# Performance work log

Measured on AMD Instinct MI355X. Metric: run time of the kernel, lower is better.

The kernel has to match this reference:

```python
import jax, jax.numpy as jnp
import numpy as np

B, T, D = 1024, 20, 50          # batch sessions, seq len (hardcoded 20), emb dim (hardcoded 50)
S1S2 = 50 * 20                  # sample1 * sample2 friend nodes (GAT src)
DEG = 50                        # avg in-degree per dst node
E = B * DEG
NUM_USERS, NUM_ITEMS = 100000, 50000


def _lstm(x, W_ih, W_hh, b_ih, b_hh):
    """PyTorch-style LSTM (gate order i,f,g,o). x: [N,T,D] -> hs: [T,N,D]."""
    N = x.shape[0]
    h0 = jnp.zeros((N, x.shape[-1]), x.dtype)
    def step(carry, xt):
        h, c = carry
        gates = xt @ W_ih.T + h @ W_hh.T + b_ih + b_hh
        i, f, g, o = jnp.split(gates, 4, axis=-1)
        c = jax.nn.sigmoid(f) * c + jax.nn.sigmoid(i) * jnp.tanh(g)
        h = jax.nn.sigmoid(o) * jnp.tanh(c)
        return (h, c), h
    (_, _), hs = jax.lax.scan(step, (h0, h0), jnp.swapaxes(x, 0, 1))
    return hs


def _gat(feat_src, feat_dst, edge_src, edge_dst, fc_W, fc_b):
    """u_dot_v -> edge_softmax (per dst) -> u_mul_e_sum -> relu(fc)."""
    n_dst = feat_dst.shape[0]
    src_e = feat_src[edge_src]                           # [E, D] gather
    score = jnp.sum(src_e * feat_dst[edge_dst], axis=-1) # [E] u_dot_v
    m = jax.ops.segment_max(score, edge_dst, num_segments=n_dst)
    ex = jnp.exp(score - m[edge_dst])
    den = jax.ops.segment_sum(ex, edge_dst, num_segments=n_dst)
    w = ex / den[edge_dst]                               # edge_softmax
    agg = jax.ops.segment_sum(w[:, None] * src_e, edge_dst, num_segments=n_dst)
    return jax.nn.relu(agg @ fc_W.T + fc_b)


def setup_inputs() -> dict:
    key = jax.random.key(0)
    ks = jax.random.split(key, 16)
    input_session = jax.random.randint(ks[0], (B, T), 0, NUM_ITEMS, dtype=jnp.int32)
    support_nodes_layer1 = jax.random.randint(ks[1], (S1S2,), 0, NUM_USERS, dtype=jnp.int32)
    support_sessions_layer1 = jax.random.randint(ks[2], (S1S2, T), 0, NUM_ITEMS, dtype=jnp.int32)
    edge_src = jax.random.randint(ks[3], (E,), 0, S1S2, dtype=jnp.int32)
    edge_dst = jnp.repeat(jnp.arange(B, dtype=jnp.int32), DEG)  # every dst has DEG edges
    s = 0.05
    user_emb = jax.random.normal(ks[4], (NUM_USERS, D), jnp.float32) * s
    item_emb = (jax.random.normal(ks[5], (NUM_ITEMS, D), jnp.float32) * s).at[0].set(0.0)  # padding_idx=0
    W_ih = jax.random.normal(ks[6], (4 * D, D), jnp.float32) * s
    W_hh = jax.random.normal(ks[7], (4 * D, D), jnp.float32) * s
    b_ih = jax.random.normal(ks[8], (4 * D,), jnp.float32) * s
    b_hh = jax.random.normal(ks[9], (4 * D,), jnp.float32) * s
    W1 = jax.random.normal(ks[10], (D, 2 * D), jnp.float32) * s
    fc_W = jax.random.normal(ks[11], (D, D), jnp.float32) * s
    fc_b = jax.random.normal(ks[12], (D,), jnp.float32) * s
    W2 = jax.random.normal(ks[13], (D, 3 * D), jnp.float32) * s
    return {"input_session": input_session, "support_nodes_layer1": support_nodes_layer1,
            "support_sessions_layer1": support_sessions_layer1, "edge_src": edge_src,
            "edge_dst": edge_dst, "user_emb": user_emb, "item_emb": item_emb,
            "W_ih": W_ih, "W_hh": W_hh, "b_ih": b_ih, "b_hh": b_hh,
            "W1": W1, "fc_W": fc_W, "fc_b": fc_b, "W2": W2}


def reference(input_session, support_nodes_layer1, support_sessions_layer1, edge_src, edge_dst,
              user_emb, item_emb, W_ih, W_hh, b_ih, b_hh, W1, fc_W, fc_b, W2):
    # current-user short-term: LSTM over session item embeddings, take last hidden
    output = _lstm(item_emb[input_session], W_ih, W_hh, b_ih, b_hh)[-1]        # [B, D]
    # friends long-term (user emb) + short-term (LSTM over friend sessions, step 0 as in source)
    long_term1 = user_emb[support_nodes_layer1]                                 # [S1S2, D]
    short_term1 = _lstm(item_emb[support_sessions_layer1], W_ih, W_hh, b_ih, b_hh)[0]  # [S1S2, D]
    ls1 = jax.nn.relu(jnp.concatenate([long_term1, short_term1], axis=-1) @ W1.T)      # [S1S2, D]
    # GAT: gather -> per-dst edge softmax -> scatter weighted sum
    gat_out = _gat(ls1, output, edge_src, edge_dst, fc_W, fc_b)                 # [B, D]
    feat = jnp.concatenate([output, gat_out], axis=-1)                          # [B, 2D]
    sr = jnp.concatenate([output, feat], axis=-1) @ W2.T                        # [B, D]
    logits = sr @ item_emb[1:].T                                                # [B, NUM_ITEMS-1]
    return logits
```

## Files before the change

kernel.cpp:

```cpp
#include <hip/hip_runtime.h>
#include <math.h>

#define D 50
#define T 20
#define BATCH 1024
#define S1S2 1000
#define DEG 50
#define NITEMS 50000
#define NLOGITS 49999
#define KPAD 64
#define SLAB 64
#define CHW 64
#define NCHN 784
#define NIPAD (NCHN * CHW)
#define LROWI 66
#define PREP_BLKS ((NIPAD * (KPAD / 2) + 255) / 256)

using bf16x8 = __attribute__((ext_vector_type(8))) __bf16;
using f32x4  = __attribute__((ext_vector_type(4))) float;

__device__ __forceinline__ float sigf(float x) { return 1.0f / (1.0f + expf(-x)); }

__device__ __forceinline__ unsigned short f2bf(float f) {
    unsigned u = __builtin_bit_cast(unsigned, f);
    u = (u + 0x7FFFu + ((u >> 16) & 1u)) >> 16;
    return (unsigned short)u;
}

__global__ __launch_bounds__(256) void fused_front_kernel(
    const int* __restrict__ sess,
    const int* __restrict__ nodes,
    const int* __restrict__ fsess,
    const float* __restrict__ user_emb,
    const float* __restrict__ item_emb,
    const float* __restrict__ W_ih,
    const float* __restrict__ W_hh,
    const float* __restrict__ b_ih,
    const float* __restrict__ b_hh,
    const float* __restrict__ W1,
    float* __restrict__ out_h,
    float* __restrict__ ls1,
    unsigned* __restrict__ item_u)
{
    const int blk = blockIdx.x;
    const int t = threadIdx.x;

    if (blk < BATCH) {
        const int b = blk;
        __shared__ float x_s[D];
        __shared__ float h_s[D];
        __shared__ float g_s[4 * D];
        __shared__ int idx_s[T];

        if (t < T) idx_s[t] = sess[b * T + t];

        float wih[D], whh[D];
        float bias = 0.f;
        if (t < 4 * D) {
            #pragma unroll
            for (int k = 0; k < D; ++k) {
                wih[k] = W_ih[t * D + k];
                whh[k] = W_hh[t * D + k];
            }
            bias = b_ih[t] + b_hh[t];
        }
        float c = 0.f;
        if (t < D) h_s[t] = 0.f;
        __syncthreads();
        if (t < D) x_s[t] = item_emb[(size_t)idx_s[0] * D + t];
        __syncthreads();

        for (int step = 0; step < T; ++step) {
            float xn = 0.f;
            if (t < D && step + 1 < T)
                xn = item_emb[(size_t)idx_s[step + 1] * D + t];
            if (t < 4 * D) {
                float g = bias;
                #pragma unroll
                for (int k = 0; k < D; ++k)
                    g += wih[k] * x_s[k] + whh[k] * h_s[k];
                g_s[t] = g;
            }
            __syncthreads();
            if (t < D) {
                float ig = sigf(g_s[t]);
                float fg = sigf(g_s[D + t]);
                float gg = tanhf(g_s[2 * D + t]);
                float og = sigf(g_s[3 * D + t]);
                c = fg * c + ig * gg;
                h_s[t] = og * tanhf(c);
                if (step + 1 < T) x_s[t] = xn;
            }
            __syncthreads();
        }
        if (t < D) out_h[b * D + t] = h_s[t];
    } else if (blk < BATCH + S1S2) {
        const int s = blk - BATCH;
        __shared__ float fx_s[D];
        __shared__ float fh_s[D];
        __shared__ float fg_s[4 * D];

        if (t < D) fx_s[t] = item_emb[(size_t)fsess[s * T] * D + t];
        __syncthreads();
        if (t < 4 * D) {
            float g = b_ih[t] + b_hh[t];
            #pragma unroll
            for (int k = 0; k < D; ++k) g += W_ih[t * D + k] * fx_s[k];
            fg_s[t] = g;
        }
        __syncthreads();
        if (t < D) {
            float ig = sigf(fg_s[t]);
            float gg = tanhf(fg_s[2 * D + t]);
            float og = sigf(fg_s[3 * D + t]);
            float c1 = ig * gg;
            fh_s[t] = og * tanhf(c1);
        }
        __syncthreads();
        if (t < D) {
            const int node = nodes[s];
            const float* ue = user_emb + (size_t)node * D;
            const float* w1r = W1 + t * 2 * D;
            float acc = 0.f;
            #pragma unroll
            for (int k = 0; k < D; ++k) acc += ue[k] * w1r[k];
            #pragma unroll
            for (int k = 0; k < D; ++k) acc += fh_s[k] * w1r[D + k];
            ls1[s * D + t] = fmaxf(acc, 0.f);
        }
    } else {
        const int idx = (blk - BATCH - S1S2) * 256 + t;
        if (idx >= NIPAD * (KPAD / 2)) return;
        const int r = idx >> 5, c2 = idx & 31;
        const int c0 = c2 * 2, c1 = c0 + 1;
        float f0 = 0.f, f1 = 0.f;
        if (r < NLOGITS) {
            const float* row = item_emb + (size_t)(1 + r) * D;
            if (c0 < D) f0 = row[c0];
            if (c1 < D) f1 = row[c1];
        }
        item_u[idx] = (unsigned)f2bf(f0) | ((unsigned)f2bf(f1) << 16);
    }
}

__global__ __launch_bounds__(64) void gat_sr_kernel(
    const float* __restrict__ out_h,
    const float* __restrict__ ls1,
    const int* __restrict__ edge_src,
    const float* __restrict__ fc_W,
    const float* __restrict__ fc_b,
    const float* __restrict__ W2,
    unsigned* __restrict__ sr_u)
{
    const int b = blockIdx.x;
    const int l = threadIdx.x;
    __shared__ float q[D];
    __shared__ int srcs[DEG];
    __shared__ float w_s[DEG];
    __shared__ float a_s[D];
    __shared__ float g_s[D];
    __shared__ float srow_s[KPAD];

    srow_s[l] = 0.f;
    if (l < D) q[l] = out_h[b * D + l];
    if (l < DEG) srcs[l] = edge_src[b * DEG + l];
    __syncthreads();

    float sc = -INFINITY;
    if (l < DEG) {
        const float* row = ls1 + (size_t)srcs[l] * D;
        float s = 0.f;
        #pragma unroll
        for (int k = 0; k < D; ++k) s += row[k] * q[k];
        sc = s;
    }
    float m = sc;
    #pragma unroll
    for (int off = 32; off; off >>= 1) m = fmaxf(m, __shfl_xor(m, off));
    float ex = (l < DEG) ? expf(sc - m) : 0.f;
    float den = ex;
    #pragma unroll
    for (int off = 32; off; off >>= 1) den += __shfl_xor(den, off);
    if (l < DEG) w_s[l] = ex / den;
    __syncthreads();

    if (l < D) {
        float a = 0.f;
        #pragma unroll
        for (int j = 0; j < DEG; ++j) a += w_s[j] * ls1[(size_t)srcs[j] * D + l];
        a_s[l] = a;
    }
    __syncthreads();
    if (l < D) {
        float g = fc_b[l];
        #pragma unroll
        for (int k = 0; k < D; ++k) g += a_s[k] * fc_W[l * D + k];
        g_s[l] = fmaxf(g, 0.f);
    }
    __syncthreads();
    if (l < D) {
        const float* w2r = W2 + l * 3 * D;
        float v = 0.f;
        #pragma unroll
        for (int k = 0; k < D; ++k) v += q[k] * (w2r[k] + w2r[D + k]);
        #pragma unroll
        for (int k = 0; k < D; ++k) v += g_s[k] * w2r[2 * D + k];
        srow_s[l] = v;
    }
    __syncthreads();
    if (l < KPAD / 2) {
        unsigned u = (unsigned)f2bf(srow_s[2 * l]) |
                     ((unsigned)f2bf(srow_s[2 * l + 1]) << 16);
        sr_u[b * (KPAD / 2) + l] = u;
    }
}

__global__ __launch_bounds__(256) void logits_mfma_kernel(
    const unsigned short* __restrict__ sr_bf,
    const unsigned short* __restrict__ item_bf,
    float* __restrict__ out)
{
    const int n = blockIdx.x;
    const int slab = n / NCHN;
    const int j = n - slab * NCHN;
    const int chunk = (j & 7) * 98 + (j >> 3);

    const int t = threadIdx.x;
    const int lane = t & 63;
    const int wave = t >> 6;
    const int r16 = lane & 15;
    const int g   = lane >> 4;
    const int b0 = slab * SLAB;
    const int ibase = chunk * CHW;

    __shared__ float ls[SLAB * LROWI];

    const unsigned short* ap =
        item_bf + (size_t)(ibase + wave * 16 + r16) * KPAD + g * 8;
    bf16x8 av0 = *(const bf16x8*)(ap);
    bf16x8 av1 = *(const bf16x8*)(ap + 32);

    #pragma unroll
    for (int bt = 0; bt < 4; ++bt) {
        const unsigned short* bp = sr_bf + (size_t)(b0 + bt * 16 + r16) * KPAD + g * 8;
        bf16x8 bv0 = *(const bf16x8*)(bp);
        bf16x8 bv1 = *(const bf16x8*)(bp + 32);
        f32x4 acc = {0.f, 0.f, 0.f, 0.f};
        acc = __builtin_amdgcn_mfma_f32_16x16x32_bf16(av0, bv0, acc, 0, 0, 0);
        acc = __builtin_amdgcn_mfma_f32_16x16x32_bf16(av1, bv1, acc, 0, 0, 0);
        *(f32x4*)&ls[(bt * 16 + r16) * LROWI + wave * 16 + g * 4] = acc;
    }
    __syncthreads();

    const int i = ibase + lane;
    const bool ok = i < NLOGITS;
    #pragma unroll
    for (int p = 0; p < 16; ++p) {
        const int brow = wave * 16 + p;
        float v = ls[brow * LROWI + lane];
        if (ok) out[(size_t)(b0 + brow) * NLOGITS + i] = v;
    }
}

extern "C" void kernel_launch(void* const* d_in, const int* in_sizes, int n_in,
                              void* d_out, int out_size, void* d_ws, size_t ws_size,
                              hipStream_t stream) {
    const int*   sess      = (const int*)d_in[0];
    const int*   nodes     = (const int*)d_in[1];
    const int*   fsess     = (const int*)d_in[2];
    const int*   edge_src  = (const int*)d_in[3];
    const float* user_emb  = (const float*)d_in[5];
    const float* item_emb  = (const float*)d_in[6];
    const float* W_ih      = (const float*)d_in[7];
    const float* W_hh      = (const float*)d_in[8];
    const float* b_ih      = (const float*)d_in[9];
    const float* b_hh      = (const float*)d_in[10];
    const float* W1        = (const float*)d_in[11];
    const float* fc_W      = (const float*)d_in[12];
    const float* fc_b      = (const float*)d_in[13];
    const float* W2        = (const float*)d_in[14];
    float* out = (float*)d_out;

    char* ws = (char*)d_ws;
    float*    out_h  = (float*)(ws);
    float*    ls1    = (float*)(ws + 204800);
    unsigned* sr_u   = (unsigned*)(ws + 404800);
    unsigned* item_u = (unsigned*)(ws + 535872);

    hipLaunchKernelGGL(fused_front_kernel,
                       dim3(BATCH + S1S2 + PREP_BLKS), dim3(256), 0, stream,
                       sess, nodes, fsess, user_emb, item_emb,
                       W_ih, W_hh, b_ih, b_hh, W1, out_h, ls1, item_u);
    hipLaunchKernelGGL(gat_sr_kernel, dim3(BATCH), dim3(64), 0, stream,
                       out_h, ls1, edge_src, fc_W, fc_b, W2, sr_u);
    hipLaunchKernelGGL(logits_mfma_kernel,
                       dim3((BATCH / SLAB) * NCHN), dim3(256), 0, stream,
                       (const unsigned short*)sr_u, (const unsigned short*)item_u, out);
}
```

Before: 115.5 us.

## Restructure logits GEMM into persistent double-buffered tiles with vectorized stores

```diff
diff --git a/kernel.cpp b/kernel.cpp
--- a/kernel.cpp
+++ b/kernel.cpp
@@ -9,11 +9,13 @@
 #define NITEMS 50000
 #define NLOGITS 49999
 #define KPAD 64
-#define SLAB 64
-#define CHW 64
-#define NCHN 784
-#define NIPAD (NCHN * CHW)
-#define LROWI 66
+#define SLAB 16
+#define GROUPS 8
+#define GSPAN 6400
+#define ITERW 256
+#define NITER 25
+#define NIPAD 51200
+#define LSTR2 276
 #define PREP_BLKS ((NIPAD * (KPAD / 2) + 255) / 256)
 
 using bf16x8 = __attribute__((ext_vector_type(8))) __bf16;
@@ -221,9 +223,8 @@
     float* __restrict__ out)
 {
     const int n = blockIdx.x;
-    const int slab = n / NCHN;
-    const int j = n - slab * NCHN;
-    const int chunk = (j & 7) * 98 + (j >> 3);
+    const int slab = n >> 3;
+    const int grp  = n & 7;
 
     const int t = threadIdx.x;
     const int lane = t & 63;
@@ -231,34 +232,52 @@
     const int r16 = lane & 15;
     const int g   = lane >> 4;
     const int b0 = slab * SLAB;
-    const int ibase = chunk * CHW;
-
-    __shared__ float ls[SLAB * LROWI];
-
-    const unsigned short* ap =
-        item_bf + (size_t)(ibase + wave * 16 + r16) * KPAD + g * 8;
-    bf16x8 av0 = *(const bf16x8*)(ap);
-    bf16x8 av1 = *(const bf16x8*)(ap + 32);
-
-    #pragma unroll
-    for (int bt = 0; bt < 4; ++bt) {
-        const unsigned short* bp = sr_bf + (size_t)(b0 + bt * 16 + r16) * KPAD + g * 8;
-        bf16x8 bv0 = *(const bf16x8*)(bp);
-        bf16x8 bv1 = *(const bf16x8*)(bp + 32);
-        f32x4 acc = {0.f, 0.f, 0.f, 0.f};
-        acc = __builtin_amdgcn_mfma_f32_16x16x32_bf16(av0, bv0, acc, 0, 0, 0);
-        acc = __builtin_amdgcn_mfma_f32_16x16x32_bf16(av1, bv1, acc, 0, 0, 0);
-        *(f32x4*)&ls[(bt * 16 + r16) * LROWI + wave * 16 + g * 4] = acc;
-    }
-    __syncthreads();
-
-    const int i = ibase + lane;
-    const bool ok = i < NLOGITS;
-    #pragma unroll
-    for (int p = 0; p < 16; ++p) {
-        const int brow = wave * 16 + p;
-        float v = ls[brow * LROWI + lane];
-        if (ok) out[(size_t)(b0 + brow) * NLOGITS + i] = v;
+    const int gbase = grp * GSPAN;
+
+    __shared__ float ls[2][SLAB * LSTR2];
+
+    const unsigned short* bp = sr_bf + (size_t)(b0 + r16) * KPAD + g * 8;
+    bf16x8 bv0 = *(const bf16x8*)(bp);
+    bf16x8 bv1 = *(const bf16x8*)(bp + 32);
+
+    auto compute = [&](int it, int buf) {
+        const int ib = gbase + it * ITERW + wave * 64;
+        #pragma unroll
+        for (int m = 0; m < 4; ++m) {
+            const unsigned short* ap =
+                item_bf + (size_t)(ib + m * 16 + r16) * KPAD + g * 8;
+            bf16x8 av0 = *(const bf16x8*)(ap);
+            bf16x8 av1 = *(const bf16x8*)(ap + 32);
+            f32x4 acc = {0.f, 0.f, 0.f, 0.f};
+            acc = __builtin_amdgcn_mfma_f32_16x16x32_bf16(av0, bv0, acc, 0, 0, 0);
+            acc = __builtin_amdgcn_mfma_f32_16x16x32_bf16(av1, bv1, acc, 0, 0, 0);
+            *(f32x4*)&ls[buf][r16 * LSTR2 + wave * 64 + m * 16 + g * 4] = acc;
+        }
+    };
+
+    compute(0, 0);
+    __syncthreads();
+
+    for (int it = 0; it < NITER; ++it) {
+        const int buf = it & 1;
+        const int cbase = gbase + it * ITERW;
+        const int c = lane * 4;
+        #pragma unroll
+        for (int p = 0; p < 4; ++p) {
+            const int row = wave * 4 + p;
+            const f32x4 v = *(const f32x4*)&ls[buf][row * LSTR2 + c];
+            float* orow = out + (size_t)(b0 + row) * NLOGITS;
+            const int col = cbase + c;
+            if (col + 3 < NLOGITS) {
+                *(float4*)(orow + col) = make_float4(v[0], v[1], v[2], v[3]);
+            } else {
+                #pragma unroll
+                for (int r = 0; r < 4; ++r)
+                    if (col + r < NLOGITS) orow[col + r] = v[r];
+            }
+        }
+        if (it + 1 < NITER) compute(it + 1, buf ^ 1);
+        __syncthreads();
     }
 }
 
@@ -294,6 +313,6 @@
     hipLaunchKernelGGL(gat_sr_kernel, dim3(BATCH), dim3(64), 0, stream,
                        out_h, ls1, edge_src, fc_W, fc_b, W2, sr_u);
     hipLaunchKernelGGL(logits_mfma_kernel,
-                       dim3((BATCH / SLAB) * NCHN), dim3(256), 0, stream,
+                       dim3(64 * GROUPS), dim3(256), 0, stream,
                        (const unsigned short*)sr_u, (const unsigned short*)item_u, out);
 }
```

Result: faster. 106.2 us, median of 2 (-8.0%).
